# Kernel tuning notes

Measured on AMD Instinct MI355X. Metric: run time of the kernel, lower is better.

The kernel has to match this reference:

```python
import jax, jax.numpy as jnp
import numpy as np

N_STATE = 32  # SSM states per channel (S4D)


def lrelu(x):
    return jnp.where(x >= 0, x, 0.3 * x)


def conv1d(x, w, b, stride=1, pad=0, dil=1):
    # x: [B,C,L], w: [O,I,K]
    y = jax.lax.conv_general_dilated(
        x, w, (stride,), [(pad, pad)], rhs_dilation=(dil,),
        dimension_numbers=('NCH', 'OIH', 'NCH'))
    return y + b[None, :, None]


def batchnorm(x, g, b, eps=1e-5):
    # training-mode BatchNorm1d: stats over (B, L) per channel
    m = jnp.mean(x, axis=(0, 2), keepdims=True)
    v = jnp.var(x, axis=(0, 2), keepdims=True)
    return (x - m) * jax.lax.rsqrt(v + eps) * g[None, :, None] + b[None, :, None]


def s4_layer(u, log_dt, C2, D):
    # Diagonal S4 (S4D-Lin): u [B,H,L] -> y [B,H,L]; causal FFT conv + skip
    H, N = C2.shape[0], C2.shape[1]
    L = u.shape[-1]
    A = -0.5 + 1j * jnp.pi * jnp.arange(N, dtype=jnp.float32)            # [N]
    dtA = jnp.exp(log_dt)[:, None] * A[None, :]                          # [H,N]
    C = (C2[..., 0] + 1j * C2[..., 1]) * (jnp.exp(dtA) - 1.0) / A        # [H,N]
    vand = jnp.exp(dtA[:, :, None] * jnp.arange(L, dtype=jnp.float32))   # [H,N,L]
    K = 2.0 * jnp.real(jnp.einsum('hn,hnl->hl', C, vand))                # [H,L]
    uf = jnp.fft.rfft(u, n=2 * L)
    Kf = jnp.fft.rfft(K, n=2 * L)
    y = jnp.fft.irfft(uf * Kf[None], n=2 * L)[..., :L]
    return y + D[None, :, None] * u


def down_block(x, s4p, convs, g, b):
    # dilated residual inception down block: S4 then 4 stride-4 dilated convs
    x = s4_layer(x, *s4p)
    d1 = batchnorm(conv1d(x, convs[0][0], convs[0][1], 4, 1, 1), g, b)
    d2 = batchnorm(lrelu(conv1d(x, convs[1][0], convs[1][1], 4, 2, 2)), g, b)
    d3 = batchnorm(lrelu(conv1d(x, convs[2][0], convs[2][1], 4, 4, 4)), g, b)
    d4 = batchnorm(lrelu(conv1d(x, convs[3][0], convs[3][1], 4, 8, 8)), g, b)
    return jnp.concatenate([d1, d2, d3, d4], axis=1)


def setup_inputs() -> dict:
    key = jax.random.key(0)
    ks = iter(jax.random.split(key, 64))

    def nrm(shape, scale=1.0):
        return jax.random.normal(next(ks), shape, jnp.float32) * scale

    def logdt(H):
        lo, hi = np.log(0.001), np.log(0.1)
        return jax.random.uniform(next(ks), (H,), jnp.float32) * (hi - lo) + lo

    B, L, DIN = 16, 8192, 2
    inp = {}
    inp['x'] = nrm((B, L, DIN))
    inp['enc_w'] = nrm((64, DIN, 1), (1.0 / DIN) ** 0.5)
    inp['enc_b'] = jnp.zeros((64,), jnp.float32)
    for pfx, H in (('s4a', 64), ('s4b', 256), ('s4c', 1024)):
        inp[pfx + '_log_dt'] = logdt(H)
        inp[pfx + '_C'] = nrm((H, N_STATE, 2), 0.5 ** 0.5)
        inp[pfx + '_D'] = nrm((H,))
    for blk, C in (('b1', 64), ('b2', 256)):
        sc = (1.0 / (C * 3)) ** 0.5
        for i in range(1, 5):
            inp[f'{blk}_w{i}'] = nrm((C, C, 3), sc)
            inp[f'{blk}_b{i}'] = nrm((C,), 0.02)
    inp['bn1_g'] = jnp.ones((64,), jnp.float32)
    inp['bn1_b'] = jnp.zeros((64,), jnp.float32)
    inp['bn2_g'] = jnp.ones((256,), jnp.float32)
    inp['bn2_b'] = jnp.zeros((256,), jnp.float32)
    inp['dec1_w'] = nrm((256, 1024, 1), (1.0 / 1024) ** 0.5)
    inp['dec1_b'] = jnp.zeros((256,), jnp.float32)
    inp['dec2_w'] = nrm((1, 256, 1), (1.0 / 256) ** 0.5)
    inp['dec2_b'] = jnp.zeros((1,), jnp.float32)
    return inp


def reference(x, enc_w, enc_b,
              s4a_log_dt, s4a_C, s4a_D,
              b1_w1, b1_b1, b1_w2, b1_b2, b1_w3, b1_b3, b1_w4, b1_b4, bn1_g, bn1_b,
              s4b_log_dt, s4b_C, s4b_D,
              b2_w1, b2_b1, b2_w2, b2_b2, b2_w3, b2_b3, b2_w4, b2_b4, bn2_g, bn2_b,
              s4c_log_dt, s4c_C, s4c_D,
              dec1_w, dec1_b, dec2_w, dec2_b):
    h = conv1d(jnp.transpose(x, (0, 2, 1)), enc_w, enc_b)                 # [B,64,L]
    x1 = down_block(h, (s4a_log_dt, s4a_C, s4a_D),
                    [(b1_w1, b1_b1), (b1_w2, b1_b2), (b1_w3, b1_b3), (b1_w4, b1_b4)],
                    bn1_g, bn1_b)                                          # [B,256,L/4]
    x2 = down_block(x1, (s4b_log_dt, s4b_C, s4b_D),
                    [(b2_w1, b2_b1), (b2_w2, b2_b2), (b2_w3, b2_b3), (b2_w4, b2_b4)],
                    bn2_g, bn2_b)                                          # [B,1024,L/16]
    x3 = s4_layer(x2, s4c_log_dt, s4c_C, s4c_D)
    y = conv1d(conv1d(x3, dec1_w, dec1_b), dec2_w, dec2_b)                 # [B,1,L/16]
    ff = jnp.squeeze(y, axis=1)                                            # [B,L/16]
    return ff[..., -1:]                                                    # [B,1]
```

## Files before the change

### kernel.cpp

```cpp
#include <hip/hip_runtime.h>
#include <math.h>

#define PI_F 3.14159265358979323846f

typedef __attribute__((ext_vector_type(8))) short short8;
typedef __attribute__((ext_vector_type(4))) float f32x4;

__device__ __forceinline__ unsigned short f2bf(float f) {
    unsigned int u = __float_as_uint(f);
    unsigned int r = (u + 0x7fffu + ((u >> 16) & 1u)) >> 16;
    return (unsigned short)r;
}
__device__ __forceinline__ float bf2f(unsigned short v) {
    return __uint_as_float((unsigned int)v << 16);
}

__global__ __launch_bounds__(256) void enc_kernel(
    const float* __restrict__ x, const float* __restrict__ ew,
    const float* __restrict__ eb, unsigned short* __restrict__ u1)
{
    int idx = blockIdx.x * 256 + threadIdx.x;
    int t4 = idx & 2047;
    int b  = (idx >> 11) & 15;
    int h  = idx >> 15;
    float w0 = ew[2*h], w1 = ew[2*h+1], bb = eb[h];
    const float* xp = x + ((size_t)b*8192 + (size_t)t4*4)*2;
    float4 a = *(const float4*)xp;
    float4 c = *(const float4*)(xp + 4);
    ushort4 o;
    o.x = f2bf(fmaf(w0, a.x, fmaf(w1, a.y, bb)));
    o.y = f2bf(fmaf(w0, a.z, fmaf(w1, a.w, bb)));
    o.z = f2bf(fmaf(w0, c.x, fmaf(w1, c.y, bb)));
    o.w = f2bf(fmaf(w0, c.z, fmaf(w1, c.w, bb)));
    *(ushort4*)(u1 + ((size_t)h*16 + b)*8192 + (size_t)t4*4) = o;
}

__global__ __launch_bounds__(256) void prep_w(
    const float* __restrict__ w0, const float* __restrict__ w1,
    const float* __restrict__ w2, const float* __restrict__ w3,
    const float* __restrict__ w4, const float* __restrict__ w5,
    const float* __restrict__ w6, const float* __restrict__ w7,
    unsigned short* __restrict__ wprep)
{
    int id = blockIdx.y;
    const float* src; int Cin; size_t doff;
    switch (id) {
        case 0: src = w0; Cin = 64;  doff = 0;      break;
        case 1: src = w1; Cin = 64;  doff = 12288;  break;
        case 2: src = w2; Cin = 64;  doff = 24576;  break;
        case 3: src = w3; Cin = 64;  doff = 36864;  break;
        case 4: src = w4; Cin = 256; doff = 49152;  break;
        case 5: src = w5; Cin = 256; doff = 245760; break;
        case 6: src = w6; Cin = 256; doff = 442368; break;
        default: src = w7; Cin = 256; doff = 638976; break;
    }
    int e = blockIdx.x * 256 + threadIdx.x;
    if (e >= Cin * Cin * 3) return;
    int kb  = e / (Cin * 32);
    int rem = e - kb * (Cin * 32);
    int o   = rem >> 5;
    int kk  = rem & 31;
    int cch = kb / 6, t6 = kb % 6, k = t6 >> 1, chalf = t6 & 1;
    int c = cch * 64 + chalf * 32 + kk;
    wprep[doff + e] = f2bf(src[((size_t)o * Cin + c) * 3 + k]);
}

__global__ __launch_bounds__(128) void prep_s4(
    const float* __restrict__ log_dt, const float* __restrict__ C2,
    const float* __restrict__ Dv,
    unsigned short* __restrict__ TA, unsigned short* __restrict__ VA,
    float* __restrict__ rs, float* __restrict__ Vrs)
{
    int h = blockIdx.x, t = threadIdx.x;
    __shared__ float cn[64];
    __shared__ float sK[128];
    __shared__ unsigned short s_w[128 * 66];
    float dt = expf(log_dt[h]);
    if (t < 32) {
        int n = t;
        float e = expf(-0.5f*dt);
        float s_, c_; sincosf(PI_F*dt*n, &s_, &c_);
        float wr = e*c_, wi = e*s_;
        float ar = -0.5f, ai = PI_F*n;
        float den = 1.f/(ar*ar + ai*ai);
        float tr = wr - 1.f, ti = wi;
        float qr = (tr*ar + ti*ai)*den;
        float qi = (ti*ar - tr*ai)*den;
        float c2r = C2[((size_t)h*32+n)*2], c2i = C2[((size_t)h*32+n)*2+1];
        cn[2*n]   = 2.f*(c2r*qr - c2i*qi);
        cn[2*n+1] = 2.f*(c2r*qi + c2i*qr);
        float e128 = expf(-64.f*dt);
        float s2, c2v; sincosf(PI_F*dt*n*128.f, &s2, &c2v);
        float pr = 1.f - e128*c2v, pim = -e128*s2;
        float dr = 1.f - wr, di = -wi;
        float dd = 1.f/(dr*dr + di*di);
        Vrs[(size_t)h*64 + 2*n]   = (pr*dr + pim*di)*dd;
        Vrs[(size_t)h*64 + 2*n+1] = (pim*dr - pr*di)*dd;
    }
    __syncthreads();
    {
        float em = expf(-0.5f*dt*t);
        float Kt = 0.f;
        for (int n = 0; n < 32; n++) {
            float s_, c_; sincosf(PI_F*dt*(float)(n*t), &s_, &c_);
            Kt += cn[2*n]*em*c_ - cn[2*n+1]*em*s_;
        }
        sK[t] = Kt + (t == 0 ? Dv[h] : 0.f);
    }
    if (t < 64) {
        int n = t >> 1, ri = t & 1;
        float e = expf(-0.5f*dt);
        float s_, c_; sincosf(PI_F*dt*n, &s_, &c_);
        float wr = e*c_, wi = e*s_;
        float crn = cn[2*n], cin = cn[2*n+1];
        float pr = wr, pim = wi;
        for (int m = 0; m < 128; m++) {
            float re = crn*pr - cin*pim;
            float im = crn*pim + cin*pr;
            s_w[m*66 + t] = f2bf(ri ? -im : re);
            float nr = pr*wr - pim*wi;
            float ni = pr*wi + pim*wr;
            pr = nr; pim = ni;
        }
    } else {
        int r = t - 64; int n = r >> 1, ri = r & 1;
        float e = expf(-0.5f*dt);
        float s_, c_; sincosf(PI_F*dt*n, &s_, &c_);
        float wr = e*c_, wi = e*s_;
        float cr2 = 1.f, ci2 = 0.f;
        for (int kb = 3; kb >= 0; kb--) {
            unsigned short buf[32];
            for (int kk = 31; kk >= 0; kk--) {
                buf[kk] = f2bf(ri ? ci2 : cr2);
                float nr = cr2*wr - ci2*wi;
                float ni = cr2*wi + ci2*wr;
                cr2 = nr; ci2 = ni;
            }
            uint4* dst = (uint4*)&VA[(((size_t)h*4 + kb)*64 + r)*32];
            uint4* src = (uint4*)buf;
            dst[0]=src[0]; dst[1]=src[1]; dst[2]=src[2]; dst[3]=src[3];
        }
    }
    __syncthreads();
    {
        float acc = 0.f;
        for (int tau = 0; tau <= t; tau++) acc += sK[tau];
        rs[(size_t)h*128 + t] = acc;
    }
    for (int kb = 0; kb < 4; kb++) {
        unsigned short tb[32];
#pragma unroll
        for (int kk = 0; kk < 32; kk++) {
            int col = kb*32 + kk;
            tb[kk] = f2bf((col <= t) ? sK[t - col] : 0.f);
        }
        uint4* dst = (uint4*)&TA[(((size_t)h*6 + kb)*128 + t)*32];
        uint4* src = (uint4*)tb;
        dst[0]=src[0]; dst[1]=src[1]; dst[2]=src[2]; dst[3]=src[3];
    }
    for (int i = t; i < 1024; i += 128) {
        int kb = i >> 9;
        int rem = i & 511;
        int m = rem >> 2, kkg = rem & 3;
        *(uint4*)&TA[(((size_t)h*6 + 4 + kb)*128 + m)*32 + kkg*8] =
            *(const uint4*)&s_w[m*66 + kb*32 + kkg*8];
    }
}

template<int NCH, int LOGNCH>
__global__ __launch_bounds__(256) void s4_layer_fused(
    const unsigned short* __restrict__ u, const unsigned short* __restrict__ VA,
    const float* __restrict__ Vrs, const unsigned short* __restrict__ TA,
    const float* __restrict__ rs, const float* __restrict__ sc,
    const float* __restrict__ sh, const float* __restrict__ log_dt,
    unsigned short* __restrict__ yout)
{
    const int L = NCH * 128;
    __shared__ unsigned short s_u[64*200];
    __shared__ unsigned short s_s[64*72];
    __shared__ float sE[64*68];
    int h = blockIdx.y;
    int tid = threadIdx.x;
    int lane = tid & 63, wid = tid >> 6;
    int nl = lane & 15, g = lane >> 4;
    int col0 = blockIdx.x * 64;
    float scv = sc ? sc[h] : 1.f;
    float shv = sh ? sh[h] : 0.f;

    for (int i = tid; i < 1024; i += 256) {
        int cl = i >> 4, o = i & 15;
        int col = col0 + cl; int b = col >> LOGNCH, c = col & (NCH - 1);
        *(uint4*)&s_u[cl*200 + o*8] =
            *(const uint4*)&u[((size_t)h*16 + b)*L + c*128 + o*8];
    }
    __syncthreads();

    {
        int cl = wid*16 + nl;
        f32x4 acc[4];
#pragma unroll
        for (int mt = 0; mt < 4; mt++) acc[mt] = (f32x4){0.f,0.f,0.f,0.f};
#pragma unroll
        for (int kb = 0; kb < 4; kb++) {
            short8 bf = *(const short8*)&s_u[cl*200 + kb*32 + g*8];
#pragma unroll
            for (int mt = 0; mt < 4; mt++) {
                short8 af = *(const short8*)(VA + (((size_t)h*4 + kb)*64 + mt*16 + nl)*32 + g*8);
                acc[mt] = __builtin_amdgcn_mfma_f32_16x16x32_bf16(af, bf, acc[mt], 0, 0, 0);
            }
        }
#pragma unroll
        for (int mt = 0; mt < 4; mt++) {
            int j0 = mt*16 + g*4;
            float4 vr = *(const float4*)(Vrs + (size_t)h*64 + j0);
            sE[cl*68 + j0 + 0] = fmaf(scv, acc[mt][0], shv*vr.x);
            sE[cl*68 + j0 + 1] = fmaf(scv, acc[mt][1], shv*vr.y);
            sE[cl*68 + j0 + 2] = fmaf(scv, acc[mt][2], shv*vr.z);
            sE[cl*68 + j0 + 3] = fmaf(scv, acc[mt][3], shv*vr.w);
        }
    }
    __syncthreads();

    constexpr int NB = 64 / NCH;
    if (tid < NB * 32) {
        int bl = tid >> 5, n = tid & 31;
        float dt = expf(log_dt[h]);
        float e = expf(-0.5f * dt);
        float s_, c_; sincosf(PI_F * dt * n, &s_, &c_);
        float Wr = e*c_, Wi = e*s_;
#pragma unroll
        for (int i = 0; i < 7; i++) { float r = Wr*Wr - Wi*Wi; float im = 2.f*Wr*Wi; Wr = r; Wi = im; }
        float Sr = 0.f, Si = 0.f;
        for (int c2 = 0; c2 < NCH; c2++) {
            float* ep = &sE[(bl*NCH + c2)*68 + 2*n];
            float er = ep[0], ei = ep[1];
            ep[0] = Sr; ep[1] = Si;
            float r  = fmaf(Wr, Sr, fmaf(-Wi, Si, er));
            float im = fmaf(Wi, Sr, fmaf( Wr, Si, ei));
            Sr = r; Si = im;
        }
    }
    __syncthreads();

    for (int i = tid*4; i < 4096; i += 1024) {
        int cl = i >> 6, j = i & 63;
        ushort4 q;
        q.x = f2bf(sE[cl*68 + j]);
        q.y = f2bf(sE[cl*68 + j+1]);
        q.z = f2bf(sE[cl*68 + j+2]);
        q.w = f2bf(sE[cl*68 + j+3]);
        *(ushort4*)&s_s[cl*72 + j] = q;
    }
    __syncthreads();

    f32x4 accT[2][4], accW[2][4];
#pragma unroll
    for (int a = 0; a < 2; a++)
#pragma unroll
        for (int j = 0; j < 4; j++) { accT[a][j] = (f32x4){0,0,0,0}; accW[a][j] = (f32x4){0,0,0,0}; }
#pragma unroll
    for (int kb = 0; kb < 4; kb++) {
        short8 bfr[4];
#pragma unroll
        for (int j = 0; j < 4; j++)
            bfr[j] = *(const short8*)&s_u[(j*16 + nl)*200 + kb*32 + g*8];
#pragma unroll
        for (int mt2 = 0; mt2 < 2; mt2++) {
            int mtile = wid*2 + mt2;
            short8 af = *(const short8*)&TA[(((size_t)h*6 + kb)*128 + mtile*16 + nl)*32 + g*8];
#pragma unroll
            for (int j = 0; j < 4; j++)
                accT[mt2][j] = __builtin_amdgcn_mfma_f32_16x16x32_bf16(af, bfr[j], accT[mt2][j], 0, 0, 0);
        }
    }
#pragma unroll
    for (int kw = 0; kw < 2; kw++) {
        short8 bfr[4];
#pragma unroll
        for (int j = 0; j < 4; j++)
            bfr[j] = *(const short8*)&s_s[(j*16 + nl)*72 + kw*32 + g*8];
#pragma unroll
        for (int mt2 = 0; mt2 < 2; mt2++) {
            int mtile = wid*2 + mt2;
            short8 af = *(const short8*)&TA[(((size_t)h*6 + 4 + kw)*128 + mtile*16 + nl)*32 + g*8];
#pragma unroll
            for (int j = 0; j < 4; j++)
                accW[mt2][j] = __builtin_amdgcn_mfma_f32_16x16x32_bf16(af, bfr[j], accW[mt2][j], 0, 0, 0);
        }
    }
#pragma unroll
    for (int mt2 = 0; mt2 < 2; mt2++) {
        int m0 = (wid*2 + mt2)*16 + g*4;
        float4 rsv = *(const float4*)&rs[(size_t)h*128 + m0];
#pragma unroll
        for (int j = 0; j < 4; j++) {
            int col = col0 + j*16 + nl; int b = col >> LOGNCH, c = col & (NCH - 1);
            ushort4 q;
            q.x = f2bf(fmaf(scv, accT[mt2][j][0], shv*rsv.x) + accW[mt2][j][0]);
            q.y = f2bf(fmaf(scv, accT[mt2][j][1], shv*rsv.y) + accW[mt2][j][1]);
            q.z = f2bf(fmaf(scv, accT[mt2][j][2], shv*rsv.z) + accW[mt2][j][2]);
            q.w = f2bf(fmaf(scv, accT[mt2][j][3], shv*rsv.w) + accW[mt2][j][3]);
            *(ushort4*)&yout[((size_t)h*16 + b)*L + c*128 + m0] = q;
        }
    }
}

template<int CIN, int TBLK>
__global__ __launch_bounds__(256, 2) void conv_mfma4(
    const unsigned short* __restrict__ u, const unsigned short* __restrict__ wp,
    const float* __restrict__ bs0, const float* __restrict__ bs1,
    const float* __restrict__ bs2, const float* __restrict__ bs3,
    unsigned short* __restrict__ out, int Lin, int Lout)
{
    constexpr int F     = TBLK / 16;
    constexpr int NPOS  = TBLK * 4 + 16;
    constexpr int Q     = NPOS / 4;
    constexpr int NITEM = (NPOS / 8) * 64;
    constexpr int NLD   = (NITEM + 255) / 256;
    constexpr int NCC   = CIN / 64;
    constexpr int NBUF  = (NCC > 1) ? 2 : 1;
    constexpr int BUFSZ = 4 * Q * 64;
    __shared__ unsigned short s_in[NBUF * BUFSZ];

    int tid = threadIdx.x;
    int lane = tid & 63, wid = tid >> 6;
    int nl = lane & 15, g = lane >> 4;
    int t0 = blockIdx.x * TBLK;
    int b  = blockIdx.y;
    int og = blockIdx.z * 64;
    const int P0 = t0 * 4 - 8;
    const int DIL = 1 << wid;

    f32x4 acc[4][F];
#pragma unroll
    for (int m = 0; m < 4; m++)
#pragma unroll
        for (int f = 0; f < F; f++) acc[m][f] = (f32x4){0.f,0.f,0.f,0.f};

    uint4 stg[NLD];

    auto stage_load = [&](int ccbase) {
#pragma unroll
        for (int j = 0; j < NLD; j++) {
            int i = tid + 256 * j;
            uint4 v; v.x = 0u; v.y = 0u; v.z = 0u; v.w = 0u;
            if (i < NITEM) {
                int ch = i & 63, po = i >> 6;
                int p = P0 + po * 8;
                const unsigned short* gp = u + ((size_t)(ccbase + ch)*16 + b)*Lin;
                if (p >= 0 && p + 8 <= Lin) {
                    v = *(const uint4*)(gp + p);
                } else {
                    alignas(16) unsigned short t8[8];
#pragma unroll
                    for (int j2 = 0; j2 < 8; j2++) {
                        int pj = p + j2;
                        t8[j2] = ((unsigned)pj < (unsigned)Lin) ? gp[pj] : (unsigned short)0;
                    }
                    v = *(const uint4*)t8;
                }
            }
            stg[j] = v;
        }
    };
    auto stage_write = [&](int bufidx) {
        unsigned short* sb = s_in + bufidx * BUFSZ;
#pragma unroll
        for (int j = 0; j < NLD; j++) {
            int i = tid + 256 * j;
            if (i < NITEM) {
                int ch = i & 63, po = i >> 6;
                alignas(16) unsigned short t8[8];
                *(uint4*)t8 = stg[j];
#pragma unroll
                for (int jj = 0; jj < 8; jj++) {
                    int pl = po * 8 + jj;
                    int row = (pl & 3) * Q + (pl >> 2);
                    sb[row * 64 + (ch ^ ((row & 7) << 3))] = t8[jj];
                }
            }
        }
    };

    stage_load(0);
    stage_write(0);
    __syncthreads();

#pragma unroll
    for (int cc = 0; cc < NCC; cc++) {
        if (cc + 1 < NCC) stage_load((cc + 1) * 64);
        const unsigned short* sb = s_in + (NBUF > 1 ? (cc & 1) * BUFSZ : 0);
#pragma unroll
        for (int k = 0; k < 3; ++k) {
            const int off = (k - 1) * DIL + 8;
            const int r = off & 3, s = off >> 2;
#pragma unroll
            for (int chalf = 0; chalf < 2; ++chalf) {
                int kb = cc * 6 + k * 2 + chalf;
                short8 bfr[F];
#pragma unroll
                for (int f = 0; f < F; ++f) {
                    int q = f*16 + nl + s;
                    int row = r * Q + q;
                    bfr[f] = *(const short8*)&sb[row * 64 +
                        ((((chalf << 2) | g) ^ (row & 7)) << 3)];
                }
#pragma unroll
                for (int m = 0; m < 4; ++m) {
                    short8 afrag = *(const short8*)&wp[(size_t)wid*(3*CIN*CIN) +
                        ((size_t)kb*CIN + og + m*16 + nl)*32 + g*8];
#pragma unroll
                    for (int f = 0; f < F; ++f)
                        acc[m][f] = __builtin_amdgcn_mfma_f32_16x16x32_bf16(afrag, bfr[f], acc[m][f], 0, 0, 0);
                }
            }
        }
        if (cc + 1 < NCC) {
            __syncthreads();
            stage_write((cc + 1) & 1);
            __syncthreads();
        }
    }

    const float* bp = (wid == 0) ? bs0 : (wid == 1) ? bs1 : (wid == 2) ? bs2 : bs3;
#pragma unroll
    for (int m = 0; m < 4; ++m) {
#pragma unroll
        for (int f = 0; f < F; ++f) {
            int t = t0 + f*16 + nl;
#pragma unroll
            for (int r2 = 0; r2 < 4; ++r2) {
                int o = og + m*16 + g*4 + r2;
                float v = acc[m][f][r2] + bp[o];
                if (wid) v = v >= 0.f ? v : 0.3f*v;
                out[((size_t)(wid*CIN + o)*16 + b)*Lout + t] = f2bf(v);
            }
        }
    }
}

__global__ __launch_bounds__(256) void bn_stats(
    const unsigned short* __restrict__ x, const float* __restrict__ g,
    const float* __restrict__ bb, float* __restrict__ sc, float* __restrict__ sh,
    int n, int gmask)
{
    int ch = blockIdx.x;
    const unsigned short* xp = x + (size_t)ch * n;
    float s1 = 0.f, s2 = 0.f;
    for (int i = threadIdx.x*8; i < n; i += 2048) {
        uint4 raw = *(const uint4*)(xp + i);
        unsigned short us[8]; *(uint4*)us = raw;
#pragma unroll
        for (int j = 0; j < 8; j++) {
            float v = bf2f(us[j]);
            s1 += v; s2 += v*v;
        }
    }
    for (int o = 32; o > 0; o >>= 1) { s1 += __shfl_down(s1, o); s2 += __shfl_down(s2, o); }
    __shared__ float p1[4], p2[4];
    int wid = threadIdx.x >> 6;
    if ((threadIdx.x & 63) == 0) { p1[wid] = s1; p2[wid] = s2; }
    __syncthreads();
    if (threadIdx.x == 0) {
        s1 = p1[0] + p1[1] + p1[2] + p1[3];
        s2 = p2[0] + p2[1] + p2[2] + p2[3];
        float m = s1 / n;
        float var = s2 / n - m*m;
        float rstd = rsqrtf(var + 1e-5f);
        float scale = g[ch & gmask] * rstd;
        sc[ch] = scale;
        sh[ch] = fmaf(-m, scale, bb[ch & gmask]);
    }
}

__global__ __launch_bounds__(64) void s4c_all(
    const unsigned short* __restrict__ u,
    const float* __restrict__ sc, const float* __restrict__ sh,
    const float* __restrict__ log_dt, const float* __restrict__ C2,
    const float* __restrict__ Dv, float* __restrict__ x3last)
{
    __shared__ float sE[64 * 68];
    __shared__ float red[16 * 33];
    __shared__ unsigned short sVA[4 * 64 * 32];
    __shared__ alignas(16) float sVrs[64];
    int h = blockIdx.x;
    int lane = threadIdx.x;
    int nl = lane & 15, g = lane >> 4;
    float scv = sc[h], shv = sh[h];
    float dt = expf(log_dt[h]);

    {
        int t = lane, n = t >> 1, ri = t & 1;
        float e = expf(-0.5f*dt);
        float s_, c_; sincosf(PI_F*dt*n, &s_, &c_);
        float wr = e*c_, wi = e*s_;
        float cr2 = 1.f, ci2 = 0.f;
        int key = (t >> 1) & 3;
        for (int kb = 3; kb >= 0; kb--) {
            alignas(16) unsigned short buf[32];
            for (int kk = 31; kk >= 0; kk--) {
                buf[kk] = f2bf(ri ? ci2 : cr2);
                float nr = cr2*wr - ci2*wi;
                float ni = cr2*wi + ci2*wr;
                cr2 = nr; ci2 = ni;
            }
            uint4* dst = (uint4*)&sVA[(kb*64 + t)*32];
            uint4* src4 = (uint4*)buf;
#pragma unroll
            for (int cc = 0; cc < 4; cc++) dst[cc ^ key] = src4[cc];
        }
        if (ri == 0) {
            float e128 = expf(-64.f*dt);
            float s2, c2v; sincosf(PI_F*dt*n*128.f, &s2, &c2v);
            float pr = 1.f - e128*c2v, pim = -e128*s2;
            float dr = 1.f - wr, di = -wi;
            float dd = 1.f/(dr*dr + di*di);
            sVrs[2*n]   = (pr*dr + pim*di)*dd;
            sVrs[2*n+1] = (pim*dr - pr*di)*dd;
        }
    }
    __syncthreads();

    int rkey = (nl >> 1) & 3;
    for (int cg = 0; cg < 4; cg++) {
        int col = cg*16 + nl;
        int b = col >> 2, c = col & 3;
        const unsigned short* up = u + ((size_t)h*16 + b)*512 + c*128;
        f32x4 acc[4];
#pragma unroll
        for (int mt = 0; mt < 4; mt++) acc[mt] = (f32x4){0.f,0.f,0.f,0.f};
#pragma unroll
        for (int kb = 0; kb < 4; kb++) {
            short8 bf = *(const short8*)(up + kb*32 + g*8);
#pragma unroll
            for (int mt = 0; mt < 4; mt++) {
                short8 af = *(const short8*)&sVA[(kb*64 + mt*16 + nl)*32 + ((g ^ rkey) << 3)];
                acc[mt] = __builtin_amdgcn_mfma_f32_16x16x32_bf16(af, bf, acc[mt], 0, 0, 0);
            }
        }
#pragma unroll
        for (int mt = 0; mt < 4; mt++) {
            int j0 = mt*16 + g*4;
            float4 vr = *(const float4*)&sVrs[j0];
            sE[col*68 + j0 + 0] = fmaf(scv, acc[mt][0], shv*vr.x);
            sE[col*68 + j0 + 1] = fmaf(scv, acc[mt][1], shv*vr.y);
            sE[col*68 + j0 + 2] = fmaf(scv, acc[mt][2], shv*vr.z);
            sE[col*68 + j0 + 3] = fmaf(scv, acc[mt][3], shv*vr.w);
        }
    }
    __syncthreads();

    int n = lane >> 1, bh = lane & 1;
    float e = expf(-0.5f * dt);
    float s_, c_; sincosf(PI_F * dt * n, &s_, &c_);
    float wr = e*c_, wi = e*s_;
    float ar = -0.5f, ai = PI_F * n;
    float den = 1.f / (ar*ar + ai*ai);
    float tr = wr - 1.f, ti = wi;
    float qr = (tr*ar + ti*ai) * den;
    float qi = (ti*ar - tr*ai) * den;
    float c2r = C2[((size_t)h*32 + n)*2], c2i = C2[((size_t)h*32 + n)*2 + 1];
    float crv = c2r*qr - c2i*qi, civ = c2r*qi + c2i*qr;
    float Wr = wr, Wi = wi;
#pragma unroll
    for (int i = 0; i < 7; i++) { float r = Wr*Wr - Wi*Wi; float im = 2.f*Wr*Wi; Wr = r; Wi = im; }
#pragma unroll
    for (int b2 = 0; b2 < 8; b2++) {
        int b = bh*8 + b2;
        float Sr = 0.f, Si = 0.f;
#pragma unroll
        for (int c = 0; c < 4; c++) {
            int col = b*4 + c;
            float er = sE[col*68 + 2*n], ei = sE[col*68 + 2*n + 1];
            float r  = fmaf(Wr, Sr, fmaf(-Wi, Si, er));
            float im = fmaf(Wi, Sr, fmaf( Wr, Si, ei));
            Sr = r; Si = im;
        }
        red[b*33 + n] = crv*Sr - civ*Si;
    }
    __syncthreads();
    if (lane < 16) {
        int b = lane;
        float s = 0.f;
        for (int n2 = 0; n2 < 32; n2++) s += red[b*33 + n2];
        float uv = fmaf(scv, bf2f(u[((size_t)h*16 + b)*512 + 511]), shv);
        x3last[b*1024 + h] = 2.f*s + Dv[h]*uv;
    }
}

__global__ __launch_bounds__(256) void dec_kernel(
    const float* __restrict__ x3last, const float* __restrict__ w1, const float* __restrict__ b1,
    const float* __restrict__ w2, const float* __restrict__ b2, float* __restrict__ out)
{
    __shared__ float xs[1024];
    int b = blockIdx.x, tid = threadIdx.x;
    for (int i = tid; i < 1024; i += 256) xs[i] = x3last[b*1024 + i];
    __syncthreads();
    float z = b1[tid];
    const float* wpt = w1 + (size_t)tid*1024;
    for (int i = 0; i < 1024; i += 4) {
        float4 wv = *(const float4*)(wpt + i);
        z = fmaf(wv.x, xs[i],   z);
        z = fmaf(wv.y, xs[i+1], z);
        z = fmaf(wv.z, xs[i+2], z);
        z = fmaf(wv.w, xs[i+3], z);
    }
    float v = w2[tid] * z;
    for (int o = 32; o > 0; o >>= 1) v += __shfl_down(v, o);
    __shared__ float ps[4];
    if ((tid & 63) == 0) ps[tid >> 6] = v;
    __syncthreads();
    if (tid == 0) out[b] = ps[0] + ps[1] + ps[2] + ps[3] + b2[0];
}

extern "C" void kernel_launch(void* const* d_in, const int* in_sizes, int n_in,
                              void* d_out, int out_size, void* d_ws, size_t ws_size,
                              hipStream_t stream)
{
    const float* x       = (const float*)d_in[0];
    const float* enc_w   = (const float*)d_in[1];
    const float* enc_b   = (const float*)d_in[2];
    const float* s4a_ldt = (const float*)d_in[3];
    const float* s4a_C   = (const float*)d_in[4];
    const float* s4a_D   = (const float*)d_in[5];
    const float* s4b_ldt = (const float*)d_in[6];
    const float* s4b_C   = (const float*)d_in[7];
    const float* s4b_D   = (const float*)d_in[8];
    const float* s4c_ldt = (const float*)d_in[9];
    const float* s4c_C   = (const float*)d_in[10];
    const float* s4c_D   = (const float*)d_in[11];
    const float* b1w[4] = {(const float*)d_in[12], (const float*)d_in[14], (const float*)d_in[16], (const float*)d_in[18]};
    const float* b1b[4] = {(const float*)d_in[13], (const float*)d_in[15], (const float*)d_in[17], (const float*)d_in[19]};
    const float* b2w[4] = {(const float*)d_in[20], (const float*)d_in[22], (const float*)d_in[24], (const float*)d_in[26]};
    const float* b2b[4] = {(const float*)d_in[21], (const float*)d_in[23], (const float*)d_in[25], (const float*)d_in[27]};
    const float* bn1_g  = (const float*)d_in[28];
    const float* bn1_b  = (const float*)d_in[29];
    const float* bn2_g  = (const float*)d_in[30];
    const float* bn2_b  = (const float*)d_in[31];
    const float* dec1_w = (const float*)d_in[32];
    const float* dec1_b = (const float*)d_in[33];
    const float* dec2_w = (const float*)d_in[34];
    const float* dec2_b = (const float*)d_in[35];
    float* out = (float*)d_out;

    char* ws = (char*)d_ws;
    unsigned short* u1    = (unsigned short*)(ws);
    unsigned short* u3    = u1;
    unsigned short* ya    = (unsigned short*)(ws + 16777216);
    unsigned short* yb    = ya;
    unsigned short* u2    = (unsigned short*)(ws + 33554432);
    unsigned short* wprep = (unsigned short*)(ws + 88080384);
    unsigned short* TA_a  = (unsigned short*)(ws + 89751552);
    unsigned short* TA_b  = (unsigned short*)(ws + 92897280);
    unsigned short* VA_a  = (unsigned short*)(ws + 105480192);
    unsigned short* VA_b  = (unsigned short*)(ws + 106528768);
    float*          rs_a  = (float*)(ws + 110723072);
    float*          rs_b  = (float*)(ws + 110755840);
    float*          Vrs_a = (float*)(ws + 110886912);
    float*          Vrs_b = (float*)(ws + 110903296);
    float*          smallp= (float*)(ws + 110968832);
    float* sc1 = smallp;
    float* sh1 = smallp + 256;
    float* sc2 = smallp + 512;
    float* sh2 = smallp + 1536;
    float* x3l = smallp + 2560;

    prep_w<<<dim3(768, 8), 256, 0, stream>>>(b1w[0], b1w[1], b1w[2], b1w[3],
                                             b2w[0], b2w[1], b2w[2], b2w[3], wprep);
    prep_s4<<<64, 128, 0, stream>>>(s4a_ldt, s4a_C, s4a_D, TA_a, VA_a, rs_a, Vrs_a);
    prep_s4<<<256, 128, 0, stream>>>(s4b_ldt, s4b_C, s4b_D, TA_b, VA_b, rs_b, Vrs_b);

    enc_kernel<<<8192, 256, 0, stream>>>(x, enc_w, enc_b, u1);

    s4_layer_fused<64,6><<<dim3(16, 64), 256, 0, stream>>>(
        u1, VA_a, Vrs_a, TA_a, rs_a, nullptr, nullptr, s4a_ldt, ya);

    conv_mfma4<64,32><<<dim3(64, 16, 1), 256, 0, stream>>>(
        ya, wprep, b1b[0], b1b[1], b1b[2], b1b[3], u2, 8192, 2048);
    bn_stats<<<256, 256, 0, stream>>>(u2, bn1_g, bn1_b, sc1, sh1, 16*2048, 63);

    s4_layer_fused<16,4><<<dim3(4, 256), 256, 0, stream>>>(
        u2, VA_b, Vrs_b, TA_b, rs_b, sc1, sh1, s4b_ldt, yb);

    conv_mfma4<256,64><<<dim3(8, 16, 4), 256, 0, stream>>>(
        yb, wprep + 49152, b2b[0], b2b[1], b2b[2], b2b[3], u3, 2048, 512);
    bn_stats<<<1024, 256, 0, stream>>>(u3, bn2_g, bn2_b, sc2, sh2, 16*512, 255);

    s4c_all<<<1024, 64, 0, stream>>>(u3, sc2, sh2, s4c_ldt, s4c_C, s4c_D, x3l);

    dec_kernel<<<16, 256, 0, stream>>>(x3l, dec1_w, dec1_b, dec2_w, dec2_b, out);
}
```

Baseline: 325.7 us.

## Fuse encoder into first S4 layer, merge S4 prep, widen s4c block

The pointwise encoder conv is now computed inside the first S4 layer's shared-memory load, so the bf16 u1 tensor is never written to or read back from global memory, and one launch goes away. The two prep_s4 launches become a single launch covering both layers. s4c_all moves from one wave to four: each wave builds one k-block of the Vandermonde table (starting from a directly computed power) and one column group of the MFMA work. In exchange, the raw input is re-read once per channel inside the S4 kernel, and s4c_all's serial reduction phase leaves three waves idle.

```diff
diff --git a/kernel.cpp b/kernel.cpp
--- a/kernel.cpp
+++ b/kernel.cpp
@@ -13,26 +13,6 @@
 }
 __device__ __forceinline__ float bf2f(unsigned short v) {
     return __uint_as_float((unsigned int)v << 16);
-}
-
-__global__ __launch_bounds__(256) void enc_kernel(
-    const float* __restrict__ x, const float* __restrict__ ew,
-    const float* __restrict__ eb, unsigned short* __restrict__ u1)
-{
-    int idx = blockIdx.x * 256 + threadIdx.x;
-    int t4 = idx & 2047;
-    int b  = (idx >> 11) & 15;
-    int h  = idx >> 15;
-    float w0 = ew[2*h], w1 = ew[2*h+1], bb = eb[h];
-    const float* xp = x + ((size_t)b*8192 + (size_t)t4*4)*2;
-    float4 a = *(const float4*)xp;
-    float4 c = *(const float4*)(xp + 4);
-    ushort4 o;
-    o.x = f2bf(fmaf(w0, a.x, fmaf(w1, a.y, bb)));
-    o.y = f2bf(fmaf(w0, a.z, fmaf(w1, a.w, bb)));
-    o.z = f2bf(fmaf(w0, c.x, fmaf(w1, c.y, bb)));
-    o.w = f2bf(fmaf(w0, c.z, fmaf(w1, c.w, bb)));
-    *(ushort4*)(u1 + ((size_t)h*16 + b)*8192 + (size_t)t4*4) = o;
 }
 
 __global__ __launch_bounds__(256) void prep_w(
@@ -65,13 +45,21 @@
     wprep[doff + e] = f2bf(src[((size_t)o * Cin + c) * 3 + k]);
 }
 
-__global__ __launch_bounds__(128) void prep_s4(
-    const float* __restrict__ log_dt, const float* __restrict__ C2,
-    const float* __restrict__ Dv,
-    unsigned short* __restrict__ TA, unsigned short* __restrict__ VA,
-    float* __restrict__ rs, float* __restrict__ Vrs)
+__global__ __launch_bounds__(128) void prep_s4_both(
+    const float* __restrict__ ldt_a, const float* __restrict__ C2_a,
+    const float* __restrict__ Dv_a,
+    unsigned short* __restrict__ TA_a, unsigned short* __restrict__ VA_a,
+    float* __restrict__ rs_a, float* __restrict__ Vrs_a,
+    const float* __restrict__ ldt_b, const float* __restrict__ C2_b,
+    const float* __restrict__ Dv_b,
+    unsigned short* __restrict__ TA_b, unsigned short* __restrict__ VA_b,
+    float* __restrict__ rs_b, float* __restrict__ Vrs_b)
 {
-    int h = blockIdx.x, t = threadIdx.x;
+    int bid = blockIdx.x, t = threadIdx.x;
+    const float* log_dt; const float* C2; const float* Dv;
+    unsigned short* TA; unsigned short* VA; float* rs; float* Vrs; int h;
+    if (bid < 64) { h = bid;      log_dt = ldt_a; C2 = C2_a; Dv = Dv_a; TA = TA_a; VA = VA_a; rs = rs_a; Vrs = Vrs_a; }
+    else          { h = bid - 64; log_dt = ldt_b; C2 = C2_b; Dv = Dv_b; TA = TA_b; VA = VA_b; rs = rs_b; Vrs = Vrs_b; }
     __shared__ float cn[64];
     __shared__ float sK[128];
     __shared__ unsigned short s_w[128 * 66];
@@ -167,9 +155,11 @@
     }
 }
 
-template<int NCH, int LOGNCH>
+template<int NCH, int LOGNCH, bool ENC>
 __global__ __launch_bounds__(256) void s4_layer_fused(
-    const unsigned short* __restrict__ u, const unsigned short* __restrict__ VA,
+    const unsigned short* __restrict__ u, const float* __restrict__ xg,
+    const float* __restrict__ ew, const float* __restrict__ ebv,
+    const unsigned short* __restrict__ VA,
     const float* __restrict__ Vrs, const unsigned short* __restrict__ TA,
     const float* __restrict__ rs, const float* __restrict__ sc,
     const float* __restrict__ sh, const float* __restrict__ log_dt,
@@ -187,11 +177,35 @@
     float scv = sc ? sc[h] : 1.f;
     float shv = sh ? sh[h] : 0.f;
 
-    for (int i = tid; i < 1024; i += 256) {
-        int cl = i >> 4, o = i & 15;
-        int col = col0 + cl; int b = col >> LOGNCH, c = col & (NCH - 1);
-        *(uint4*)&s_u[cl*200 + o*8] =
-            *(const uint4*)&u[((size_t)h*16 + b)*L + c*128 + o*8];
+    if constexpr (ENC) {
+        float w0e = ew[2*h], w1e = ew[2*h+1], bbe = ebv[h];
+        for (int i = tid; i < 1024; i += 256) {
+            int cl = i >> 4, o = i & 15;
+            int col = col0 + cl; int b = col >> LOGNCH, c = col & (NCH - 1);
+            const float* xp = xg + ((size_t)b*8192 + (size_t)(c*128 + o*8))*2;
+            float4 a0 = *(const float4*)xp;
+            float4 a1 = *(const float4*)(xp + 4);
+            float4 a2 = *(const float4*)(xp + 8);
+            float4 a3 = *(const float4*)(xp + 12);
+            ushort4 q0, q1;
+            q0.x = f2bf(fmaf(w0e, a0.x, fmaf(w1e, a0.y, bbe)));
+            q0.y = f2bf(fmaf(w0e, a0.z, fmaf(w1e, a0.w, bbe)));
+            q0.z = f2bf(fmaf(w0e, a1.x, fmaf(w1e, a1.y, bbe)));
+            q0.w = f2bf(fmaf(w0e, a1.z, fmaf(w1e, a1.w, bbe)));
+            q1.x = f2bf(fmaf(w0e, a2.x, fmaf(w1e, a2.y, bbe)));
+            q1.y = f2bf(fmaf(w0e, a2.z, fmaf(w1e, a2.w, bbe)));
+            q1.z = f2bf(fmaf(w0e, a3.x, fmaf(w1e, a3.y, bbe)));
+            q1.w = f2bf(fmaf(w0e, a3.z, fmaf(w1e, a3.w, bbe)));
+            *(ushort4*)&s_u[cl*200 + o*8]     = q0;
+            *(ushort4*)&s_u[cl*200 + o*8 + 4] = q1;
+        }
+    } else {
+        for (int i = tid; i < 1024; i += 256) {
+            int cl = i >> 4, o = i & 15;
+            int col = col0 + cl; int b = col >> LOGNCH, c = col & (NCH - 1);
+            *(uint4*)&s_u[cl*200 + o*8] =
+                *(const uint4*)&u[((size_t)h*16 + b)*L + c*128 + o*8];
+        }
     }
     __syncthreads();
 
@@ -473,7 +487,7 @@
     }
 }
 
-__global__ __launch_bounds__(64) void s4c_all(
+__global__ __launch_bounds__(256) void s4c_all(
     const unsigned short* __restrict__ u,
     const float* __restrict__ sc, const float* __restrict__ sh,
     const float* __restrict__ log_dt, const float* __restrict__ C2,
@@ -484,32 +498,35 @@
     __shared__ unsigned short sVA[4 * 64 * 32];
     __shared__ alignas(16) float sVrs[64];
     int h = blockIdx.x;
-    int lane = threadIdx.x;
+    int tid = threadIdx.x;
+    int lane = tid & 63, wid = tid >> 6;
     int nl = lane & 15, g = lane >> 4;
     float scv = sc[h], shv = sh[h];
     float dt = expf(log_dt[h]);
 
     {
         int t = lane, n = t >> 1, ri = t & 1;
+        int kb = wid;
         float e = expf(-0.5f*dt);
         float s_, c_; sincosf(PI_F*dt*n, &s_, &c_);
         float wr = e*c_, wi = e*s_;
-        float cr2 = 1.f, ci2 = 0.f;
+        int e0 = 96 - kb*32;
+        float em0 = expf(-0.5f*dt*(float)e0);
+        float s0, c0; sincosf(PI_F*dt*(float)n*(float)e0, &s0, &c0);
+        float cr2 = em0*c0, ci2 = em0*s0;
+        alignas(16) unsigned short buf[32];
+        for (int kk = 31; kk >= 0; kk--) {
+            buf[kk] = f2bf(ri ? ci2 : cr2);
+            float nr = cr2*wr - ci2*wi;
+            float ni = cr2*wi + ci2*wr;
+            cr2 = nr; ci2 = ni;
+        }
         int key = (t >> 1) & 3;
-        for (int kb = 3; kb >= 0; kb--) {
-            alignas(16) unsigned short buf[32];
-            for (int kk = 31; kk >= 0; kk--) {
-                buf[kk] = f2bf(ri ? ci2 : cr2);
-                float nr = cr2*wr - ci2*wi;
-                float ni = cr2*wi + ci2*wr;
-                cr2 = nr; ci2 = ni;
-            }
-            uint4* dst = (uint4*)&sVA[(kb*64 + t)*32];
-            uint4* src4 = (uint4*)buf;
-#pragma unroll
-            for (int cc = 0; cc < 4; cc++) dst[cc ^ key] = src4[cc];
-        }
-        if (ri == 0) {
+        uint4* dst = (uint4*)&sVA[(kb*64 + t)*32];
+        uint4* src4 = (uint4*)buf;
+#pragma unroll
+        for (int cc = 0; cc < 4; cc++) dst[cc ^ key] = src4[cc];
+        if (wid == 0 && ri == 0) {
             float e128 = expf(-64.f*dt);
             float s2, c2v; sincosf(PI_F*dt*n*128.f, &s2, &c2v);
             float pr = 1.f - e128*c2v, pim = -e128*s2;
@@ -522,8 +539,8 @@
     __syncthreads();
 
     int rkey = (nl >> 1) & 3;
-    for (int cg = 0; cg < 4; cg++) {
-        int col = cg*16 + nl;
+    {
+        int col = wid*16 + nl;
         int b = col >> 2, c = col & 3;
         const unsigned short* up = u + ((size_t)h*16 + b)*512 + c*128;
         f32x4 acc[4];
@@ -550,37 +567,39 @@
     }
     __syncthreads();
 
-    int n = lane >> 1, bh = lane & 1;
-    float e = expf(-0.5f * dt);
-    float s_, c_; sincosf(PI_F * dt * n, &s_, &c_);
-    float wr = e*c_, wi = e*s_;
-    float ar = -0.5f, ai = PI_F * n;
-    float den = 1.f / (ar*ar + ai*ai);
-    float tr = wr - 1.f, ti = wi;
-    float qr = (tr*ar + ti*ai) * den;
-    float qi = (ti*ar - tr*ai) * den;
-    float c2r = C2[((size_t)h*32 + n)*2], c2i = C2[((size_t)h*32 + n)*2 + 1];
-    float crv = c2r*qr - c2i*qi, civ = c2r*qi + c2i*qr;
-    float Wr = wr, Wi = wi;
-#pragma unroll
-    for (int i = 0; i < 7; i++) { float r = Wr*Wr - Wi*Wi; float im = 2.f*Wr*Wi; Wr = r; Wi = im; }
-#pragma unroll
-    for (int b2 = 0; b2 < 8; b2++) {
-        int b = bh*8 + b2;
-        float Sr = 0.f, Si = 0.f;
-#pragma unroll
-        for (int c = 0; c < 4; c++) {
-            int col = b*4 + c;
-            float er = sE[col*68 + 2*n], ei = sE[col*68 + 2*n + 1];
-            float r  = fmaf(Wr, Sr, fmaf(-Wi, Si, er));
-            float im = fmaf(Wi, Sr, fmaf( Wr, Si, ei));
-            Sr = r; Si = im;
-        }
-        red[b*33 + n] = crv*Sr - civ*Si;
-    }
-    __syncthreads();
-    if (lane < 16) {
-        int b = lane;
+    if (tid < 64) {
+        int n = lane >> 1, bh = lane & 1;
+        float e = expf(-0.5f * dt);
+        float s_, c_; sincosf(PI_F * dt * n, &s_, &c_);
+        float wr = e*c_, wi = e*s_;
+        float ar = -0.5f, ai = PI_F * n;
+        float den = 1.f / (ar*ar + ai*ai);
+        float tr = wr - 1.f, ti = wi;
+        float qr = (tr*ar + ti*ai) * den;
+        float qi = (ti*ar - tr*ai) * den;
+        float c2r = C2[((size_t)h*32 + n)*2], c2i = C2[((size_t)h*32 + n)*2 + 1];
+        float crv = c2r*qr - c2i*qi, civ = c2r*qi + c2i*qr;
+        float Wr = wr, Wi = wi;
+#pragma unroll
+        for (int i = 0; i < 7; i++) { float r = Wr*Wr - Wi*Wi; float im = 2.f*Wr*Wi; Wr = r; Wi = im; }
+#pragma unroll
+        for (int b2 = 0; b2 < 8; b2++) {
+            int b = bh*8 + b2;
+            float Sr = 0.f, Si = 0.f;
+#pragma unroll
+            for (int c = 0; c < 4; c++) {
+                int col = b*4 + c;
+                float er = sE[col*68 + 2*n], ei = sE[col*68 + 2*n + 1];
+                float r  = fmaf(Wr, Sr, fmaf(-Wi, Si, er));
+                float im = fmaf(Wi, Sr, fmaf( Wr, Si, ei));
+                Sr = r; Si = im;
+            }
+            red[b*33 + n] = crv*Sr - civ*Si;
+        }
+    }
+    __syncthreads();
+    if (tid < 16) {
+        int b = tid;
         float s = 0.f;
         for (int n2 = 0; n2 < 32; n2++) s += red[b*33 + n2];
         float uv = fmaf(scv, bf2f(u[((size_t)h*16 + b)*512 + 511]), shv);
@@ -644,8 +663,7 @@
     float* out = (float*)d_out;
 
     char* ws = (char*)d_ws;
-    unsigned short* u1    = (unsigned short*)(ws);
-    unsigned short* u3    = u1;
+    unsigned short* u3    = (unsigned short*)(ws);
     unsigned short* ya    = (unsigned short*)(ws + 16777216);
     unsigned short* yb    = ya;
     unsigned short* u2    = (unsigned short*)(ws + 33554432);
@@ -667,26 +685,25 @@
 
     prep_w<<<dim3(768, 8), 256, 0, stream>>>(b1w[0], b1w[1], b1w[2], b1w[3],
                                              b2w[0], b2w[1], b2w[2], b2w[3], wprep);
-    prep_s4<<<64, 128, 0, stream>>>(s4a_ldt, s4a_C, s4a_D, TA_a, VA_a, rs_a, Vrs_a);
-    prep_s4<<<256, 128, 0, stream>>>(s4b_ldt, s4b_C, s4b_D, TA_b, VA_b, rs_b, Vrs_b);
-
-    enc_kernel<<<8192, 256, 0, stream>>>(x, enc_w, enc_b, u1);
-
-    s4_layer_fused<64,6><<<dim3(16, 64), 256, 0, stream>>>(
-        u1, VA_a, Vrs_a, TA_a, rs_a, nullptr, nullptr, s4a_ldt, ya);
+    prep_s4_both<<<320, 128, 0, stream>>>(
+        s4a_ldt, s4a_C, s4a_D, TA_a, VA_a, rs_a, Vrs_a,
+        s4b_ldt, s4b_C, s4b_D, TA_b, VA_b, rs_b, Vrs_b);
+
+    s4_layer_fused<64,6,true><<<dim3(16, 64), 256, 0, stream>>>(
+        nullptr, x, enc_w, enc_b, VA_a, Vrs_a, TA_a, rs_a, nullptr, nullptr, s4a_ldt, ya);
 
     conv_mfma4<64,32><<<dim3(64, 16, 1), 256, 0, stream>>>(
         ya, wprep, b1b[0], b1b[1], b1b[2], b1b[3], u2, 8192, 2048);
     bn_stats<<<256, 256, 0, stream>>>(u2, bn1_g, bn1_b, sc1, sh1, 16*2048, 63);
 
-    s4_layer_fused<16,4><<<dim3(4, 256), 256, 0, stream>>>(
-        u2, VA_b, Vrs_b, TA_b, rs_b, sc1, sh1, s4b_ldt, yb);
+    s4_layer_fused<16,4,false><<<dim3(4, 256), 256, 0, stream>>>(
+        u2, nullptr, nullptr, nullptr, VA_b, Vrs_b, TA_b, rs_b, sc1, sh1, s4b_ldt, yb);
 
     conv_mfma4<256,64><<<dim3(8, 16, 4), 256, 0, stream>>>(
         yb, wprep + 49152, b2b[0], b2b[1], b2b[2], b2b[3], u3, 2048, 512);
     bn_stats<<<1024, 256, 0, stream>>>(u3, bn2_g, bn2_b, sc2, sh2, 16*512, 255);
 
-    s4c_all<<<1024, 64, 0, stream>>>(u3, sc2, sh2, s4c_ldt, s4c_C, s4c_D, x3l);
+    s4c_all<<<1024, 256, 0, stream>>>(u3, sc2, sh2, s4c_ldt, s4c_C, s4c_D, x3l);
 
     dec_kernel<<<16, 256, 0, stream>>>(x3l, dec1_w, dec1_b, dec2_w, dec2_b, out);
 }
```

After: 302.4 us. -7.1%, faster.
